# Performance work log

Hardware: AMD Instinct MI355X
Metric: run time of the kernel (lower is better)

## Reference

```python
import jax, jax.numpy as jnp
import numpy as np

B, S, IN_DIM, P_DIM, H = 2, 2048, 1024, 512, 8
HD = P_DIM // H
N_PENTA = 1024
SCALES = (128, 256, 512)
K_NEIGH = max(16, min(int(S * 0.15), 128))  # adaptive window -> 128
SCALE = 1.0 / float(np.sqrt(HD))
EPS = 1e-5


def _ln(x, g, b):
    mu = jnp.mean(x, axis=-1, keepdims=True)
    var = jnp.mean((x - mu) ** 2, axis=-1, keepdims=True)
    return (x - mu) * jax.lax.rsqrt(var + EPS) * g + b


def setup_inputs() -> dict:
    key = jax.random.key(0)
    ks = list(jax.random.split(key, 6 + 2 * len(SCALES)))
    w = lambda k, shp: jax.random.normal(k, shp, jnp.float32) * 0.02
    inp = {
        'sequence_features': jax.random.normal(ks[0], (B, S, IN_DIM), jnp.float32),
        'shared_pentachora': jax.random.normal(ks[1], (N_PENTA, 5, P_DIM), jnp.float32),
        'shared_positions': jax.random.uniform(ks[2], (N_PENTA,), dtype=jnp.float32),
        'proj_W': w(ks[3], (IN_DIM, P_DIM)), 'proj_b': jnp.zeros((P_DIM,), jnp.float32),
        'ln_g': jnp.ones((P_DIM,), jnp.float32), 'ln_b': jnp.zeros((P_DIM,), jnp.float32),
        'qkv_W': w(ks[4], (P_DIM, 3 * P_DIM)), 'qkv_b': jnp.zeros((3 * P_DIM,), jnp.float32),
        'out_W': w(ks[5], (P_DIM, P_DIM)), 'out_b': jnp.zeros((P_DIM,), jnp.float32),
    }
    i = 6
    for s in SCALES:
        inp[f'w1_{s}'] = w(ks[i], (P_DIM, 2 * s)); inp[f'b1_{s}'] = jnp.zeros((2 * s,), jnp.float32)
        inp[f'g_{s}'] = jnp.ones((2 * s,), jnp.float32); inp[f'bb_{s}'] = jnp.zeros((2 * s,), jnp.float32)
        inp[f'w2_{s}'] = w(ks[i + 1], (2 * s, s)); inp[f'b2_{s}'] = jnp.zeros((s,), jnp.float32)
        i += 2
    return inp


def _attend_one(z_b, pos_b, qkv_W, qkv_b, out_W, out_b):
    # z_b: [S, P_DIM], pos_b: [S]
    qkv = (z_b @ qkv_W + qkv_b).reshape(S, 3, H, HD)
    q = jnp.transpose(qkv[:, 0], (1, 0, 2))  # [H, S, HD]
    k = jnp.transpose(qkv[:, 1], (1, 0, 2))
    v = jnp.transpose(qkv[:, 2], (1, 0, 2))
    dist = jnp.abs(pos_b[:, None] - pos_b[None, :])  # [S, S]
    _, routes = jax.lax.top_k(-dist, K_NEIGH)        # [S, K] nearest in Cantor space
    kg = k[:, routes, :]  # [H, S, K, HD] gathered keys
    vg = v[:, routes, :]
    scores = jnp.einsum('hqd,hqkd->hqk', q, kg) * SCALE
    attn = jax.nn.softmax(scores, axis=-1)
    out = jnp.einsum('hqk,hqkd->hqd', attn, vg)
    out = jnp.transpose(out, (1, 0, 2)).reshape(S, P_DIM)
    return out @ out_W + out_b


def reference(sequence_features, shared_pentachora, shared_positions, proj_W, proj_b, ln_g, ln_b, qkv_W, qkv_b, out_W, out_b, w1_128, b1_128, g_128, bb_128, w2_128, b2_128, w1_256, b1_256, g_256, bb_256, w2_256, b2_256, w1_512, b1_512, g_512, bb_512, w2_512, b2_512):
    # centroids from pentachora vertices, L2-normalized
    cent = shared_pentachora.mean(axis=1)
    cent = cent / jnp.clip(jnp.linalg.norm(cent, axis=-1, keepdims=True), 1e-12)
    # input projection -> LN -> GELU -> L2 normalize
    z = jax.nn.gelu(_ln(sequence_features @ proj_W + proj_b, ln_g, ln_b), approximate=False)
    z = z / jnp.clip(jnp.linalg.norm(z, axis=-1, keepdims=True), 1e-12)
    # match to opinion anchors, inherit Cantor positions
    anchor_ids = jnp.argmax(jnp.einsum('bnd,pd->bnp', z, cent), axis=-1)  # [B, S]
    cantor_positions = shared_positions[anchor_ids]  # [B, S]
    # per-sample geometric sparse attention (vmapped over batch)
    z_att = jax.vmap(_attend_one, in_axes=(0, 0, None, None, None, None))(
        z, cantor_positions, qkv_W, qkv_b, out_W, out_b)  # [B, S, P_DIM]
    pooled = z_att.mean(axis=1)  # [B, P_DIM] (no attention mask)
    scale_params = (
        (w1_128, b1_128, g_128, bb_128, w2_128, b2_128),
        (w1_256, b1_256, g_256, bb_256, w2_256, b2_256),
        (w1_512, b1_512, g_512, bb_512, w2_512, b2_512),
    )
    outs = []
    for (w1, b1, g, bb, w2, b2) in scale_params:
        h = jax.nn.gelu(_ln(pooled @ w1 + b1, g, bb), approximate=False)
        outs.append(h @ w2 + b2)
    return jnp.concatenate(outs, axis=-1)  # [B, 128+256+512] concatenated scale opinions
```

## Files before the change

### kernel.cpp

```cpp
#include <hip/hip_runtime.h>
#include <math.h>

#define DEV __device__ __forceinline__

static constexpr int S_LEN  = 2048;
static constexpr int IN_DIM = 1024;
static constexpr int P_DIM  = 512;
static constexpr int NHEAD  = 8;
static constexpr int HD     = 64;
static constexpr int KN     = 128;

typedef __attribute__((ext_vector_type(8))) short bf16x8;
typedef __attribute__((ext_vector_type(4))) float f32x4;

DEV float gelu_exact(float x) {
    return 0.5f * x * (1.0f + erff(x * 0.70710678118654752440f));
}

DEV short bf_hi(float x) {
    unsigned u = __float_as_uint(x);
    unsigned r = (u + 0x7fffu + ((u >> 16) & 1u)) >> 16;
    return (short)r;
}
DEV float bf_f(short h) { return __uint_as_float(((unsigned)(unsigned short)h) << 16); }

DEV float block_reduce_sum(float v, float* sm4) {
    #pragma unroll
    for (int off = 32; off; off >>= 1) v += __shfl_down(v, off, 64);
    int lane = threadIdx.x & 63, w = threadIdx.x >> 6;
    __syncthreads();
    if (lane == 0) sm4[w] = v;
    __syncthreads();
    return sm4[0] + sm4[1] + sm4[2] + sm4[3];
}

__global__ __launch_bounds__(256) void k_split(const float* __restrict__ X,
                                               short* __restrict__ Xh,
                                               short* __restrict__ Xl) {
    long base = ((long)blockIdx.x * 256 + threadIdx.x) * 16;
    #pragma unroll
    for (int u = 0; u < 4; u++) {
        float4 v = *(const float4*)(X + base + u * 4);
        short h0 = bf_hi(v.x), h1 = bf_hi(v.y), h2 = bf_hi(v.z), h3 = bf_hi(v.w);
        *(short4*)(Xh + base + u * 4) = make_short4(h0, h1, h2, h3);
        *(short4*)(Xl + base + u * 4) =
            make_short4(bf_hi(v.x - bf_f(h0)), bf_hi(v.y - bf_f(h1)),
                        bf_hi(v.z - bf_f(h2)), bf_hi(v.w - bf_f(h3)));
    }
}

__global__ __launch_bounds__(256) void k_cent(const float* __restrict__ penta,
                                              short* __restrict__ ch,
                                              short* __restrict__ cl) {
    int p = blockIdx.x, t = threadIdx.x;
    __shared__ float sm4[4];
    float c0 = 0.f, c1 = 0.f;
    #pragma unroll
    for (int v = 0; v < 5; v++) {
        const float* row = penta + ((long)p * 5 + v) * P_DIM;
        c0 += row[t];
        c1 += row[t + 256];
    }
    c0 /= 5.0f; c1 /= 5.0f;
    float tot = block_reduce_sum(c0 * c0 + c1 * c1, sm4);
    float n = fmaxf(sqrtf(tot), 1e-12f);
    float v0 = c0 / n, v1 = c1 / n;
    short h0 = bf_hi(v0), h1 = bf_hi(v1);
    ch[p * P_DIM + t]       = h0;
    ch[p * P_DIM + t + 256] = h1;
    cl[p * P_DIM + t]       = bf_hi(v0 - bf_f(h0));
    cl[p * P_DIM + t + 256] = bf_hi(v1 - bf_f(h1));
}

template <int K, int N>
__global__ __launch_bounds__(256) void k_wt(const float* __restrict__ W,
                                            short* __restrict__ WTh,
                                            short* __restrict__ WTl) {
    __shared__ float tile[64][65];
    int bk = blockIdx.x, bn = blockIdx.y;
    int t = threadIdx.x;
    int c = t & 63, r4 = t >> 6;
    #pragma unroll
    for (int i = 0; i < 16; i++) {
        int row = r4 + i * 4;
        tile[row][c] = W[(long)(bk * 64 + row) * N + bn * 64 + c];
    }
    __syncthreads();
    #pragma unroll
    for (int i = 0; i < 16; i++) {
        int n = r4 + i * 4;
        float v = tile[c][n];
        short h = bf_hi(v);
        long o = (long)(bn * 64 + n) * K + bk * 64 + c;
        WTh[o] = h;
        WTl[o] = bf_hi(v - bf_f(h));
    }
}

template <int BM, int K, int N, int EPI>
__global__ __launch_bounds__(256) void k_mm(const short* __restrict__ Ash,
                                            const short* __restrict__ Asl,
                                            const short* __restrict__ BTh,
                                            const short* __restrict__ BTl,
                                            const float* __restrict__ bias,
                                            float* __restrict__ C,
                                            unsigned long long* __restrict__ rowkey) {
    constexpr int TI  = BM / 32;
    constexpr int CA  = BM / 8;
    constexpr int NCH = 2 * CA + 32;
    __shared__ __align__(128) short AhS[BM * 64], AlS[BM * 64];
    __shared__ __align__(128) short BhS[128 * 64], BlS[128 * 64];
    int t = threadIdx.x;
    int lane = t & 63, wave = t >> 6;
    int wr = (wave >> 1) * (BM / 2), wc = (wave & 1) * 64;
    int m = lane & 15, quad = lane >> 4;
    int rb = blockIdx.x * BM, cb = blockIdx.y * 128;
    int r8 = lane >> 3, p8 = lane & 7;
    int sl = p8 ^ r8;

    f32x4 acc[TI][4];
    #pragma unroll
    for (int i = 0; i < TI; i++)
        #pragma unroll
        for (int j = 0; j < 4; j++) acc[i][j] = (f32x4){0.f, 0.f, 0.f, 0.f};

    for (int k0 = 0; k0 < K; k0 += 64) {
        __syncthreads();
        for (int c = wave; c < NCH; c += 4) {
            const short* src; short* dst;
            if (c < CA) {
                src = Ash + (long)(rb + c * 8 + r8) * K + k0 + sl * 8;
                dst = AhS + c * 512;
            } else if (c < 2 * CA) {
                int cc = c - CA;
                src = Asl + (long)(rb + cc * 8 + r8) * K + k0 + sl * 8;
                dst = AlS + cc * 512;
            } else if (c < 2 * CA + 16) {
                int cc = c - 2 * CA;
                src = BTh + (long)(cb + cc * 8 + r8) * K + k0 + sl * 8;
                dst = BhS + cc * 512;
            } else {
                int cc = c - 2 * CA - 16;
                src = BTl + (long)(cb + cc * 8 + r8) * K + k0 + sl * 8;
                dst = BlS + cc * 512;
            }
            __builtin_amdgcn_global_load_lds(
                (const __attribute__((address_space(1))) unsigned int*)src,
                (__attribute__((address_space(3))) unsigned int*)dst, 16, 0, 0);
        }
        __syncthreads();

        #pragma unroll
        for (int ks = 0; ks < 2; ks++) {
            int so = ((ks * 4 + quad) ^ (m & 7)) * 8;
            bf16x8 ah[TI], al[TI], bh[4], bl[4];
            #pragma unroll
            for (int i = 0; i < TI; i++) {
                int off = (wr + i * 16 + m) * 64 + so;
                ah[i] = *(const bf16x8*)(AhS + off);
                al[i] = *(const bf16x8*)(AlS + off);
            }
            #pragma unroll
            for (int j = 0; j < 4; j++) {
                int off = (wc + j * 16 + m) * 64 + so;
                bh[j] = *(const bf16x8*)(BhS + off);
                bl[j] = *(const bf16x8*)(BlS + off);
            }
            #pragma unroll
            for (int i = 0; i < TI; i++)
                #pragma unroll
                for (int j = 0; j < 4; j++) {
                    acc[i][j] = __builtin_amdgcn_mfma_f32_16x16x32_bf16(ah[i], bh[j], acc[i][j], 0, 0, 0);
                    acc[i][j] = __builtin_amdgcn_mfma_f32_16x16x32_bf16(ah[i], bl[j], acc[i][j], 0, 0, 0);
                    acc[i][j] = __builtin_amdgcn_mfma_f32_16x16x32_bf16(al[i], bh[j], acc[i][j], 0, 0, 0);
                }
        }
    }

    if (EPI == 0) {
        #pragma unroll
        for (int i = 0; i < TI; i++) {
            int gr0 = rb + wr + i * 16 + quad * 4;
            #pragma unroll
            for (int j = 0; j < 4; j++) {
                int gc = cb + wc + j * 16 + m;
                float bv = bias[gc];
                #pragma unroll
                for (int r = 0; r < 4; r++)
                    C[(long)(gr0 + r) * N + gc] = acc[i][j][r] + bv;
            }
        }
    } else {
        #pragma unroll
        for (int i = 0; i < TI; i++) {
            #pragma unroll
            for (int r = 0; r < 4; r++) {
                int gr = rb + wr + i * 16 + quad * 4 + r;
                float bv = acc[i][0][r];
                int bp = cb + wc + m;
                #pragma unroll
                for (int j = 1; j < 4; j++) {
                    float v = acc[i][j][r];
                    int p = cb + wc + j * 16 + m;
                    if (v > bv) { bv = v; bp = p; }
                }
                #pragma unroll
                for (int off = 1; off < 16; off <<= 1) {
                    float ov = __shfl_xor(bv, off, 64);
                    int op = __shfl_xor(bp, off, 64);
                    if (ov > bv || (ov == bv && op < bp)) { bv = ov; bp = op; }
                }
                if (m == 0) {
                    unsigned u = __float_as_uint(bv);
                    u = (u & 0x80000000u) ? ~u : (u | 0x80000000u);
                    unsigned long long key =
                        ((unsigned long long)u << 32) | (unsigned)(0xFFFFFFFFu - (unsigned)bp);
                    atomicMax(&rowkey[gr], key);
                }
            }
        }
    }
}

__global__ __launch_bounds__(256) void k_ln_gelu_norm(const float* __restrict__ Zin,
                                                      const float* __restrict__ g,
                                                      const float* __restrict__ b,
                                                      short* __restrict__ z_h,
                                                      short* __restrict__ z_l) {
    long row = blockIdx.x;
    int t = threadIdx.x;
    __shared__ float sm4[4];
    float x0 = Zin[row * P_DIM + t], x1 = Zin[row * P_DIM + t + 256];
    float mu = block_reduce_sum(x0 + x1, sm4) * (1.0f / P_DIM);
    float d0 = x0 - mu, d1 = x1 - mu;
    float var = block_reduce_sum(d0 * d0 + d1 * d1, sm4) * (1.0f / P_DIM);
    float rs = 1.0f / sqrtf(var + 1e-5f);
    float y0 = gelu_exact(d0 * rs * g[t] + b[t]);
    float y1 = gelu_exact(d1 * rs * g[t + 256] + b[t + 256]);
    float nn = block_reduce_sum(y0 * y0 + y1 * y1, sm4);
    float n = fmaxf(sqrtf(nn), 1e-12f);
    float v0 = y0 / n, v1 = y1 / n;
    short h0 = bf_hi(v0), h1 = bf_hi(v1);
    z_h[row * P_DIM + t]       = h0;
    z_h[row * P_DIM + t + 256] = h1;
    z_l[row * P_DIM + t]       = bf_hi(v0 - bf_f(h0));
    z_l[row * P_DIM + t + 256] = bf_hi(v1 - bf_f(h1));
}

__global__ __launch_bounds__(1024) void k_sort(const unsigned long long* __restrict__ rowkey,
                                               const float* __restrict__ spos,
                                               int* __restrict__ order,
                                               float* __restrict__ pos_srt) {
    int b = blockIdx.x, t = threadIdx.x;
    __shared__ unsigned long long key[2048];
    for (int u = 0; u < 2; u++) {
        int i = t + u * 1024;
        unsigned p = 0xFFFFFFFFu - (unsigned)(rowkey[b * 2048 + i] & 0xFFFFFFFFull);
        float pv = spos[p];
        key[i] = (((unsigned long long)__float_as_uint(pv)) << 32) | (unsigned)i;
    }
    __syncthreads();
    for (int k = 2; k <= 2048; k <<= 1) {
        for (int j = k >> 1; j > 0; j >>= 1) {
            for (int u = 0; u < 2; u++) {
                int i = t + u * 1024;
                int l = i ^ j;
                if (l > i) {
                    bool up = ((i & k) == 0);
                    unsigned long long a = key[i], c = key[l];
                    if ((a > c) == up) { key[i] = c; key[l] = a; }
                }
            }
            __syncthreads();
        }
    }
    for (int u = 0; u < 2; u++) {
        int r = t + u * 1024;
        unsigned long long kk = key[r];
        order[b * 2048 + r]   = (int)(kk & 0xffffffffu);
        pos_srt[b * 2048 + r] = __uint_as_float((unsigned)(kk >> 32));
    }
}

__global__ __launch_bounds__(256) void k_routes(const float* __restrict__ pos_srt,
                                                const int* __restrict__ order,
                                                unsigned long long* __restrict__ bmG,
                                                uint2* __restrict__ bounds) {
    int blk = blockIdx.x;
    int b = blk >> 9;
    int t = threadIdx.x;
    int lane = t & 63, wave = t >> 6;
    int r = (blk & 511) * 4 + wave;
    __shared__ float ps[2048];
    __shared__ unsigned short tk[2048];
    for (int u = 0; u < 8; u++) {
        int i = t + u * 256;
        ps[i] = pos_srt[b * 2048 + i];
        tk[i] = (unsigned short)order[b * 2048 + i];
    }
    __syncthreads();

    float pi = ps[r];
    float T = 3e38f;
    #pragma unroll
    for (int a2 = 0; a2 < 2; a2++) {
        int a = lane + a2 * 64;
        int jl = r - a, jr = r + 127 - a;
        if (jl >= 0 && jr <= 2047) {
            float dl = (a > 0)   ? (pi - ps[jl]) : 0.f;
            float dr = (a < 127) ? (ps[jr] - pi) : 0.f;
            T = fminf(T, fmaxf(dl, dr));
        }
    }
    #pragma unroll
    for (int off = 1; off < 64; off <<= 1) T = fminf(T, __shfl_xor(T, off, 64));

    int lo = 0, hi = r;
    while (lo < hi) { int mid = (lo + hi) >> 1; if (pi - ps[mid] <= T) hi = mid; else lo = mid + 1; }
    int mn = lo;
    lo = r; hi = 2047;
    while (lo < hi) { int mid = (lo + hi + 1) >> 1; if (ps[mid] - pi <= T) lo = mid; else hi = mid - 1; }
    int mx = lo;
    int Ls, Rs;
    if (T > 0.f) {
        lo = 0; hi = r;
        while (lo < hi) { int mid = (lo + hi) >> 1; if (pi - ps[mid] < T) hi = mid; else lo = mid + 1; }
        Ls = lo;
        lo = r; hi = 2047;
        while (lo < hi) { int mid = (lo + hi + 1) >> 1; if (ps[mid] - pi < T) lo = mid; else hi = mid - 1; }
        Rs = lo;
    } else { Ls = r + 1; Rs = r - 1; }

    int cnt_strict = (Rs >= Ls) ? (Rs - Ls + 1) : 0;
    int need = 128 - cnt_strict;
    int l0a, l0b, r0a, r0b;
    if (cnt_strict > 0) { l0a = mn; l0b = Ls - 1; r0a = Rs + 1; r0b = mx; }
    else                { l0a = mn; l0b = mx;     r0a = 1;      r0b = 0; }
    int nL = (l0b >= l0a) ? (l0b - l0a + 1) : 0;
    int nR = (r0b >= r0a) ? (r0b - r0a + 1) : 0;
    int tiecount = nL + nR;

    int X = 65535;
    if (need < tiecount) {
        int lo2 = 0, hi2 = 2047;
        while (lo2 < hi2) {
            int mid = (lo2 + hi2) >> 1;
            int cnt = 0;
            for (int e = lane; e < tiecount; e += 64) {
                int j = (e < nL) ? (l0a + e) : (r0a + e - nL);
                cnt += (tk[j] <= mid) ? 1 : 0;
            }
            #pragma unroll
            for (int off = 1; off < 64; off <<= 1) cnt += __shfl_xor(cnt, off, 64);
            if (cnt >= need) hi2 = mid; else lo2 = mid + 1;
        }
        X = lo2;
    }

    int qlo_loc = 1 << 30, qhi_loc = -1;
    if (lane < 32) {
        unsigned long long bits = 0;
        int j0 = lane << 6, j1 = j0 + 63;
        if (cnt_strict > 0) {
            int a0 = max(Ls, j0), a1 = min(Rs, j1);
            if (a0 <= a1) {
                int s = a0 - j0, e = a1 - j0;
                unsigned long long msk = (e - s == 63) ? ~0ull
                                       : (((1ull << (e - s + 1)) - 1) << s);
                bits |= msk;
            }
        }
        int a0 = max(l0a, j0), a1 = min(l0b, j1);
        for (int j = a0; j <= a1; j++) if (tk[j] <= X) bits |= 1ull << (j - j0);
        a0 = max(r0a, j0); a1 = min(r0b, j1);
        for (int j = a0; j <= a1; j++) if (tk[j] <= X) bits |= 1ull << (j - j0);
        if (bits) {
            qlo_loc = j0 + __builtin_ctzll(bits);
            qhi_loc = j0 + 63 - __builtin_clzll(bits);
        }
        bmG[((long)(b * 2048 + r)) * 32 + lane] = bits;
    }
    #pragma unroll
    for (int off = 1; off < 64; off <<= 1) {
        qlo_loc = min(qlo_loc, __shfl_xor(qlo_loc, off, 64));
        qhi_loc = max(qhi_loc, __shfl_xor(qhi_loc, off, 64));
    }
    if (lane == 0)
        bounds[b * 2048 + r] = make_uint2((unsigned)qlo_loc, (unsigned)qhi_loc);
}

__global__ __launch_bounds__(256) void k_kprep(const float* __restrict__ qkv,
                                               const int* __restrict__ order,
                                               short* __restrict__ Ks_h,
                                               short* __restrict__ Ks_l) {
    int b = blockIdx.y;
    int t = threadIdx.x;
    int lr = t >> 5;
    int seg = t & 31;
    int rank = blockIdx.x * 8 + lr;
    int tok = order[b * 2048 + rank];
    const float4* src = (const float4*)qkv + (long)(b * 2048 + tok) * 384 + 128 + seg * 4;
    long dsto = (long)(b * 2048 + rank) * 512 + seg * 16;
    #pragma unroll
    for (int u = 0; u < 4; u++) {
        float4 v = src[u];
        short h0 = bf_hi(v.x), h1 = bf_hi(v.y), h2 = bf_hi(v.z), h3 = bf_hi(v.w);
        *(short4*)(Ks_h + dsto + u * 4) = make_short4(h0, h1, h2, h3);
        *(short4*)(Ks_l + dsto + u * 4) =
            make_short4(bf_hi(v.x - bf_f(h0)), bf_hi(v.y - bf_f(h1)),
                        bf_hi(v.z - bf_f(h2)), bf_hi(v.w - bf_f(h3)));
    }
}

__global__ __launch_bounds__(256) void k_vprep(const float* __restrict__ qkv,
                                               const int* __restrict__ order,
                                               short* __restrict__ Vt_h) {
    __shared__ short tile[64][72];
    int rt = blockIdx.x, dt = blockIdx.y, b = blockIdx.z;
    int t = threadIdx.x;
    int lr = t >> 2;
    int q4 = t & 3;
    int tok = order[b * 2048 + rt * 64 + lr];
    const float4* src = (const float4*)qkv + (long)(b * 2048 + tok) * 384 + 256 + dt * 16;
    #pragma unroll
    for (int u = 0; u < 4; u++) {
        float4 v = src[q4 + u * 4];
        int d0 = (q4 + u * 4) * 4;
        tile[d0 + 0][lr] = bf_hi(v.x);
        tile[d0 + 1][lr] = bf_hi(v.y);
        tile[d0 + 2][lr] = bf_hi(v.z);
        tile[d0 + 3][lr] = bf_hi(v.w);
    }
    __syncthreads();
    int d = t >> 2, c4 = t & 3;
    long o = ((long)(b * 512 + dt * 64 + d)) * 2048 + rt * 64 + c4 * 16;
    #pragma unroll
    for (int j = 0; j < 4; j++)
        *(short4*)(Vt_h + o + j * 4) = make_short4(tile[d][c4 * 16 + j * 4 + 0],
                                                   tile[d][c4 * 16 + j * 4 + 1],
                                                   tile[d][c4 * 16 + j * 4 + 2],
                                                   tile[d][c4 * 16 + j * 4 + 3]);
}

__global__ __launch_bounds__(256) void k_attn(const float* __restrict__ qkv,
                                              const int* __restrict__ order,
                                              const unsigned long long* __restrict__ bmG,
                                              const uint2* __restrict__ bounds,
                                              const short* __restrict__ Ks_h,
                                              const short* __restrict__ Ks_l,
                                              const short* __restrict__ Vt_h,
                                              float* __restrict__ pooledZ) {
    __shared__ __align__(16) char smem[17280];
    short* Pt = (short*)smem;
    unsigned short* cm = (unsigned short*)(smem + 10240);
    float* Opart = (float*)smem;
    float2* ml = (float2*)(smem + 16384);
    int* sh_tok = (int*)(smem + 16896);
    int* sh_lohi = (int*)(smem + 16960);
    float2* sc = (float2*)(smem + 16968);

    int gb = blockIdx.x;
    int b  = gb >> 9;
    int qg = (gb >> 2) & 127;
    int hp = gb & 3;
    int h0 = hp * 2;
    int r0 = qg * 16;
    int t = threadIdx.x;
    int lane = t & 63, wave = t >> 6;
    int rh = wave & 1, hs = wave >> 1;
    int key = lane & 15, quad = lane >> 4;

    const float4* qkvF4 = (const float4*)qkv;

    if (t < 16) sh_tok[t] = order[b * 2048 + r0 + t];
    if (t == 0) { sh_lohi[0] = 1 << 30; sh_lohi[1] = 0; }
    #pragma unroll
    for (int u = 0; u < 8; u++) {
        int e = t + u * 256;
        int c = e >> 4, q = e & 15;
        cm[c * 16 + q] = (unsigned short)(
            (bmG[((long)(b * 2048 + r0 + q)) * 32 + (c >> 2)] >> ((c & 3) * 16)) & 0xFFFF);
    }
    __syncthreads();
    if (t < 16) {
        uint2 bd = bounds[b * 2048 + r0 + t];
        atomicMin(&sh_lohi[0], (int)bd.x);
        atomicMax(&sh_lohi[1], (int)bd.y);
    }

    bf16x8 qh[2], ql[2];
    {
        long tq = (long)(b * 2048 + sh_tok[key]) * 384;
        #pragma unroll
        for (int ks = 0; ks < 2; ks++) {
            float4 v0 = qkvF4[tq + (h0 + hs) * 16 + ks * 8 + quad * 2];
            float4 v1 = qkvF4[tq + (h0 + hs) * 16 + ks * 8 + quad * 2 + 1];
            float vv[8] = {v0.x, v0.y, v0.z, v0.w, v1.x, v1.y, v1.z, v1.w};
            #pragma unroll
            for (int j = 0; j < 8; j++) {
                short hb = bf_hi(vv[j]);
                qh[ks][j] = hb;
                ql[ks][j] = bf_hi(vv[j] - bf_f(hb));
            }
        }
    }
    __syncthreads();
    int lo = sh_lohi[0] & ~63, hi = sh_lohi[1] + 1;

    float mrow[4], lrow[4];
    f32x4 Ont[4];
    #pragma unroll
    for (int r = 0; r < 4; r++) { mrow[r] = -1e30f; lrow[r] = 0.f; }
    #pragma unroll
    for (int nt = 0; nt < 4; nt++) Ont[nt] = (f32x4){0.f, 0.f, 0.f, 0.f};

    short* PtH = Pt + wave * 1280;
    short* PtL = PtH + 640;

    int hd = h0 + hs;
    long kbase = ((long)b * 2048) * 512 + hd * 64 + quad * 8;
    long vbase = ((long)(b * 512 + hd * 64 + key)) * 2048;

    for (int c0 = lo; c0 < hi; c0 += 64) {
        int cb = c0 + rh * 32;
        if (cb >= hi) continue;
        int ch0 = cb >> 4;
        unsigned long long m0 = *(const unsigned long long*)(cm + ch0 * 16 + quad * 4);
        unsigned long long m1 = (ch0 + 1 < 128)
            ? *(const unsigned long long*)(cm + (ch0 + 1) * 16 + quad * 4) : 0ull;
        if (!__any((m0 | m1) != 0ull)) continue;

        long kr0 = kbase + (long)(cb + key) * 512;
        long kr1 = kbase + (long)(cb + 16 + key) * 512;

        f32x4 S0 = (f32x4){0.f,0.f,0.f,0.f}, S1 = (f32x4){0.f,0.f,0.f,0.f};
        #pragma unroll
        for (int ks = 0; ks < 2; ks++) {
            bf16x8 b0h = *(const bf16x8*)(Ks_h + kr0 + ks * 32);
            bf16x8 b0l = *(const bf16x8*)(Ks_l + kr0 + ks * 32);
            bf16x8 b1h = *(const bf16x8*)(Ks_h + kr1 + ks * 32);
            bf16x8 b1l = *(const bf16x8*)(Ks_l + kr1 + ks * 32);
            S0 = __builtin_amdgcn_mfma_f32_16x16x32_bf16(qh[ks], b0h, S0, 0, 0, 0);
            S0 = __builtin_amdgcn_mfma_f32_16x16x32_bf16(qh[ks], b0l, S0, 0, 0, 0);
            S0 = __builtin_amdgcn_mfma_f32_16x16x32_bf16(ql[ks], b0h, S0, 0, 0, 0);
            S1 = __builtin_amdgcn_mfma_f32_16x16x32_bf16(qh[ks], b1h, S1, 0, 0, 0);
            S1 = __builtin_amdgcn_mfma_f32_16x16x32_bf16(qh[ks], b1l, S1, 0, 0, 0);
            S1 = __builtin_amdgcn_mfma_f32_16x16x32_bf16(ql[ks], b1h, S1, 0, 0, 0);
        }
        float s0[4], s1[4], p0[4], p1[4];
        unsigned bit0[4], bit1[4];
        #pragma unroll
        for (int r = 0; r < 4; r++) {
            bit0[r] = (unsigned)((m0 >> (r * 16 + key)) & 1);
            bit1[r] = (unsigned)((m1 >> (r * 16 + key)) & 1);
            s0[r] = bit0[r] ? S0[r] * 0.125f : -1e30f;
            s1[r] = bit1[r] ? S1[r] * 0.125f : -1e30f;
        }
        #pragma unroll
        for (int r = 0; r < 4; r++) {
            float cmax = fmaxf(s0[r], s1[r]);
            cmax = fmaxf(cmax, __shfl_xor(cmax, 1, 64));
            cmax = fmaxf(cmax, __shfl_xor(cmax, 2, 64));
            cmax = fmaxf(cmax, __shfl_xor(cmax, 4, 64));
            cmax = fmaxf(cmax, __shfl_xor(cmax, 8, 64));
            float mn = fmaxf(mrow[r], cmax);
            float alpha = __expf(mrow[r] - mn);
            mrow[r] = mn;
            p0[r] = bit0[r] ? __expf(s0[r] - mn) : 0.f;
            p1[r] = bit1[r] ? __expf(s1[r] - mn) : 0.f;
            float rs = p0[r] + p1[r];
            rs += __shfl_xor(rs, 1, 64);
            rs += __shfl_xor(rs, 2, 64);
            rs += __shfl_xor(rs, 4, 64);
            rs += __shfl_xor(rs, 8, 64);
            lrow[r] = lrow[r] * alpha + rs;
            #pragma unroll
            for (int nt = 0; nt < 4; nt++) Ont[nt][r] *= alpha;
        }
        #pragma unroll
        for (int r = 0; r < 4; r++) {
            short ha = bf_hi(p0[r]);
            PtH[(quad * 4 + r) * 40 + key] = ha;
            PtL[(quad * 4 + r) * 40 + key] = bf_hi(p0[r] - bf_f(ha));
            short hb = bf_hi(p1[r]);
            PtH[(quad * 4 + r) * 40 + 16 + key] = hb;
            PtL[(quad * 4 + r) * 40 + 16 + key] = bf_hi(p1[r] - bf_f(hb));
        }
        bf16x8 pfh = *(const bf16x8*)(PtH + key * 40 + quad * 8);
        bf16x8 pfl = *(const bf16x8*)(PtL + key * 40 + quad * 8);
        #pragma unroll
        for (int nt = 0; nt < 4; nt++) {
            bf16x8 vf = *(const bf16x8*)(Vt_h + vbase + (long)nt * 16 * 2048
                                         + cb + quad * 8);
            Ont[nt] = __builtin_amdgcn_mfma_f32_16x16x32_bf16(pfh, vf, Ont[nt], 0, 0, 0);
            Ont[nt] = __builtin_amdgcn_mfma_f32_16x16x32_bf16(pfl, vf, Ont[nt], 0, 0, 0);
        }
    }

    if (key == 0) {
        #pragma unroll
        for (int r = 0; r < 4; r++)
            ml[(rh * 2 + hs) * 16 + quad * 4 + r] = make_float2(mrow[r], lrow[r]);
    }
    __syncthreads();
    #pragma unroll
    for (int nt = 0; nt < 4; nt++)
        #pragma unroll
        for (int r = 0; r < 4; r++)
            Opart[rh * 2048 + (quad * 4 + r) * 128 + hs * 64 + nt * 16 + key] = Ont[nt][r];

    if (t < 32) {
        int q = t >> 1, hs2 = t & 1;
        float2 a = ml[(0 * 2 + hs2) * 16 + q];
        float2 c = ml[(1 * 2 + hs2) * 16 + q];
        float M = fmaxf(a.x, c.x);
        float w0 = __expf(a.x - M), w1 = __expf(c.x - M);
        float inv = 1.0f / fmaxf(a.y * w0 + c.y * w1, 1e-37f);
        sc[hs2 * 16 + q] = make_float2(w0 * inv, w1 * inv);
    }
    __syncthreads();

    if (t < 128) {
        int d = t, hs2 = d >> 6;
        float s = 0.f;
        #pragma unroll
        for (int q = 0; q < 16; q++) {
            float2 w = sc[hs2 * 16 + q];
            s += Opart[q * 128 + d] * w.x + Opart[2048 + q * 128 + d] * w.y;
        }
        atomicAdd(&pooledZ[b * P_DIM + h0 * HD + d], s);
    }
}

__global__ __launch_bounds__(256) void k_opool(const float* __restrict__ pooledZ,
                                               const float* __restrict__ outW,
                                               const float* __restrict__ outb,
                                               float* __restrict__ pooled) {
    int b = blockIdx.y, t = threadIdx.x;
    int c = blockIdx.x * 256 + t;
    __shared__ float pz[P_DIM];
    pz[t]       = pooledZ[b * P_DIM + t];
    pz[t + 256] = pooledZ[b * P_DIM + t + 256];
    __syncthreads();
    float acc = 0.f;
    #pragma unroll 8
    for (int d = 0; d < P_DIM; d++) acc = fmaf(pz[d], outW[d * P_DIM + c], acc);
    pooled[b * P_DIM + c] = acc + (float)S_LEN * outb[c];
}

__global__ __launch_bounds__(256) void k_exp_fc1(const float* __restrict__ pooled,
                                                 const float* __restrict__ w1_0, const float* __restrict__ b1_0,
                                                 const float* __restrict__ w1_1, const float* __restrict__ b1_1,
                                                 const float* __restrict__ w1_2, const float* __restrict__ b1_2,
                                                 float* __restrict__ h) {
    int t = threadIdx.x, b = blockIdx.y;
    int c = blockIdx.x * 256 + t;
    __shared__ float pl[P_DIM];
    pl[t]       = pooled[b * P_DIM + t]       * (1.0f / S_LEN);
    pl[t + 256] = pooled[b * P_DIM + t + 256] * (1.0f / S_LEN);
    __syncthreads();

    const float* wp; const float* bp; int s2, j;
    if (c < 256)      { wp = w1_0; bp = b1_0; s2 = 256;  j = c; }
    else if (c < 768) { wp = w1_1; bp = b1_1; s2 = 512;  j = c - 256; }
    else              { wp = w1_2; bp = b1_2; s2 = 1024; j = c - 768; }

    const float* p = wp + j;
    float acc = 0.f;
    #pragma unroll 16
    for (int k = 0; k < P_DIM; k++) {
        acc = fmaf(pl[k], *p, acc);
        p += s2;
    }
    h[(long)b * 1792 + c] = acc + bp[j];
}

__global__ __launch_bounds__(256) void k_exp_ln(float* __restrict__ h,
                                                const float* __restrict__ g0, const float* __restrict__ bb0,
                                                const float* __restrict__ g1, const float* __restrict__ bb1,
                                                const float* __restrict__ g2, const float* __restrict__ bb2) {
    int e = blockIdx.x, b = blockIdx.y, t = threadIdx.x;
    __shared__ float sm4[4];
    const int offs[3] = {0, 256, 768};
    const int ns[3]   = {256, 512, 1024};
    const float* gs[3]  = {g0, g1, g2};
    const float* bbs[3] = {bb0, bb1, bb2};
    int n = ns[e];
    float* hp = h + (long)b * 1792 + offs[e];
    const float* g = gs[e]; const float* bb = bbs[e];

    float x[4];
    float loc = 0.f;
    for (int u = 0; u < 4; u++) {
        int j = t + u * 256;
        x[u] = (j < n) ? hp[j] : 0.f;
        loc += x[u];
    }
    float mu = block_reduce_sum(loc, sm4) / (float)n;
    loc = 0.f;
    for (int u = 0; u < 4; u++) {
        int j = t + u * 256;
        if (j < n) { float d = x[u] - mu; loc += d * d; }
    }
    float var = block_reduce_sum(loc, sm4) / (float)n;
    float rs = 1.0f / sqrtf(var + 1e-5f);
    for (int u = 0; u < 4; u++) {
        int j = t + u * 256;
        if (j < n) hp[j] = gelu_exact((x[u] - mu) * rs * g[j] + bb[j]);
    }
}

__global__ __launch_bounds__(256) void k_exp_fc2(const float* __restrict__ h,
                                                 const float* __restrict__ w2_0, const float* __restrict__ b2_0,
                                                 const float* __restrict__ w2_1, const float* __restrict__ b2_1,
                                                 const float* __restrict__ w2_2, const float* __restrict__ b2_2,
                                                 float* __restrict__ out) {
    int t = threadIdx.x, b = blockIdx.y;
    int c = blockIdx.x * 256 + t;
    __shared__ float hs[1792];
    for (int u = 0; u < 7; u++) hs[t + u * 256] = h[(long)b * 1792 + t + u * 256];
    __syncthreads();
    if (c >= 896) return;

    const float* wp; const float* bp; int s2, sN, j, off_h;
    if (c < 128)      { wp = w2_0; bp = b2_0; s2 = 256;  sN = 128; j = c;       off_h = 0; }
    else if (c < 384) { wp = w2_1; bp = b2_1; s2 = 512;  sN = 256; j = c - 128; off_h = 256; }
    else              { wp = w2_2; bp = b2_2; s2 = 1024; sN = 512; j = c - 384; off_h = 768; }

    const float* p = wp + j;
    const float* hh = hs + off_h;
    float acc = 0.f;
    #pragma unroll 16
    for (int k = 0; k < s2; k++) {
        acc = fmaf(hh[k], *p, acc);
        p += sN;
    }
    out[b * 896 + c] = acc + bp[j];
}

extern "C" void kernel_launch(void* const* d_in, const int* in_sizes, int n_in,
                              void* d_out, int out_size, void* d_ws, size_t ws_size,
                              hipStream_t stream) {
    const float* seq   = (const float*)d_in[0];
    const float* penta = (const float*)d_in[1];
    const float* spos  = (const float*)d_in[2];
    const float* projW = (const float*)d_in[3];
    const float* projb = (const float*)d_in[4];
    const float* lng   = (const float*)d_in[5];
    const float* lnb   = (const float*)d_in[6];
    const float* qkvW  = (const float*)d_in[7];
    const float* qkvb  = (const float*)d_in[8];
    const float* outW  = (const float*)d_in[9];
    const float* outb  = (const float*)d_in[10];

    float* ws      = (float*)d_ws;
    float* z_pre   = ws;
    short* z_h     = (short*)(z_pre + 2097152);
    short* z_l     = z_h + 2097152;
    float* qkv     = (float*)(z_l + 2097152);
    float* pooledZ = qkv + 6291456;
    float* pooled  = pooledZ + 4096;
    float* hbuf    = pooled + 1024;
    unsigned long long* rowkey = (unsigned long long*)(hbuf + 4096);
    float* pos_srt = (float*)(rowkey + 4096);
    int*   order   = (int*)(pos_srt + 4096);
    uint2* bounds  = (uint2*)(order + 4096);
    unsigned long long* bmG = (unsigned long long*)(bounds + 4096);
    short* cent_h  = (short*)(bmG + 131072);
    short* cent_l  = cent_h + 524288;
    short* pjWT_h  = cent_l + 524288;
    short* pjWT_l  = pjWT_h + 524288;
    short* qkWT_h  = pjWT_l + 524288;
    short* qkWT_l  = qkWT_h + 786432;

    short* seq_h = (short*)qkv;
    short* seq_l = seq_h + 4194304;
    short* Ks_h = (short*)z_pre;
    short* Ks_l = Ks_h + 2097152;
    short* Vt_h = cent_h;

    k_cent<<<1024, 256, 0, stream>>>(penta, cent_h, cent_l);
    { dim3 g(16, 8);  k_wt<IN_DIM, P_DIM><<<g, 256, 0, stream>>>(projW, pjWT_h, pjWT_l); }
    { dim3 g(8, 24);  k_wt<P_DIM, 3 * P_DIM><<<g, 256, 0, stream>>>(qkvW, qkWT_h, qkWT_l); }
    k_split<<<1024, 256, 0, stream>>>(seq, seq_h, seq_l);

    { dim3 g(64, 4);  k_mm<64, IN_DIM, P_DIM, 0><<<g, 256, 0, stream>>>(
          seq_h, seq_l, pjWT_h, pjWT_l, projb, z_pre, nullptr); }
    k_ln_gelu_norm<<<4096, 256, 0, stream>>>(z_pre, lng, lnb, z_h, z_l);

    hipMemsetAsync(rowkey, 0, 4096 * sizeof(unsigned long long), stream);
    hipMemsetAsync(pooledZ, 0, 1024 * sizeof(float), stream);
    { dim3 g(32, 8);  k_mm<128, P_DIM, 1024, 1><<<g, 256, 0, stream>>>(
          z_h, z_l, cent_h, cent_l, nullptr, nullptr, rowkey); }
    k_sort<<<2, 1024, 0, stream>>>(rowkey, spos, order, pos_srt);

    { dim3 g(32, 12); k_mm<128, P_DIM, 3 * P_DIM, 0><<<g, 256, 0, stream>>>(
          z_h, z_l, qkWT_h, qkWT_l, qkvb, qkv, nullptr); }
    k_routes<<<1024, 256, 0, stream>>>(pos_srt, order, bmG, bounds);
    { dim3 g(256, 2); k_kprep<<<g, 256, 0, stream>>>(qkv, order, Ks_h, Ks_l); }
    { dim3 g(32, 8, 2); k_vprep<<<g, 256, 0, stream>>>(qkv, order, Vt_h); }
    k_attn<<<1024, 256, 0, stream>>>(qkv, order, bmG, bounds,
                                     Ks_h, Ks_l, Vt_h, pooledZ);

    { dim3 g(2, 2); k_opool<<<g, 256, 0, stream>>>(pooledZ, outW, outb, pooled); }

    dim3 g1(7, 2);
    k_exp_fc1<<<g1, 256, 0, stream>>>(pooled,
        (const float*)d_in[11], (const float*)d_in[12],
        (const float*)d_in[17], (const float*)d_in[18],
        (const float*)d_in[23], (const float*)d_in[24], hbuf);
    dim3 g2(3, 2);
    k_exp_ln<<<g2, 256, 0, stream>>>(hbuf,
        (const float*)d_in[13], (const float*)d_in[14],
        (const float*)d_in[19], (const float*)d_in[20],
        (const float*)d_in[25], (const float*)d_in[26]);
    dim3 g3(4, 2);
    k_exp_fc2<<<g3, 256, 0, stream>>>(hbuf,
        (const float*)d_in[15], (const float*)d_in[16],
        (const float*)d_in[21], (const float*)d_in[22],
        (const float*)d_in[27], (const float*)d_in[28], (float*)d_out);
}
```

Measured before the change: 393.3 us.

## Merge prep, K/V prep and tail kernels; replace bitonic sort with rank counting

Several small launches are folded into fewer kernels. The centroid, weight-transpose and input-split kernels plus the two memsets become one prep kernel, K and V prep become one, and the out-projection and expert MLP stages become a single 1024-thread tail kernel. The 2-block bitonic sort is replaced by a 16-block rank-by-counting kernel, where each thread compares its key against all 2048 keys, removing 66 barrier stages. This cuts launch and serialization overhead, at the cost of a single-block-per-batch tail with low parallelism and O(n^2) comparisons in the rank kernel.

```diff
diff --git a/kernel.cpp b/kernel.cpp
--- a/kernel.cpp
+++ b/kernel.cpp
@@ -34,50 +34,9 @@
     return sm4[0] + sm4[1] + sm4[2] + sm4[3];
 }
 
-__global__ __launch_bounds__(256) void k_split(const float* __restrict__ X,
-                                               short* __restrict__ Xh,
-                                               short* __restrict__ Xl) {
-    long base = ((long)blockIdx.x * 256 + threadIdx.x) * 16;
-    #pragma unroll
-    for (int u = 0; u < 4; u++) {
-        float4 v = *(const float4*)(X + base + u * 4);
-        short h0 = bf_hi(v.x), h1 = bf_hi(v.y), h2 = bf_hi(v.z), h3 = bf_hi(v.w);
-        *(short4*)(Xh + base + u * 4) = make_short4(h0, h1, h2, h3);
-        *(short4*)(Xl + base + u * 4) =
-            make_short4(bf_hi(v.x - bf_f(h0)), bf_hi(v.y - bf_f(h1)),
-                        bf_hi(v.z - bf_f(h2)), bf_hi(v.w - bf_f(h3)));
-    }
-}
-
-__global__ __launch_bounds__(256) void k_cent(const float* __restrict__ penta,
-                                              short* __restrict__ ch,
-                                              short* __restrict__ cl) {
-    int p = blockIdx.x, t = threadIdx.x;
-    __shared__ float sm4[4];
-    float c0 = 0.f, c1 = 0.f;
-    #pragma unroll
-    for (int v = 0; v < 5; v++) {
-        const float* row = penta + ((long)p * 5 + v) * P_DIM;
-        c0 += row[t];
-        c1 += row[t + 256];
-    }
-    c0 /= 5.0f; c1 /= 5.0f;
-    float tot = block_reduce_sum(c0 * c0 + c1 * c1, sm4);
-    float n = fmaxf(sqrtf(tot), 1e-12f);
-    float v0 = c0 / n, v1 = c1 / n;
-    short h0 = bf_hi(v0), h1 = bf_hi(v1);
-    ch[p * P_DIM + t]       = h0;
-    ch[p * P_DIM + t + 256] = h1;
-    cl[p * P_DIM + t]       = bf_hi(v0 - bf_f(h0));
-    cl[p * P_DIM + t + 256] = bf_hi(v1 - bf_f(h1));
-}
-
-template <int K, int N>
-__global__ __launch_bounds__(256) void k_wt(const float* __restrict__ W,
-                                            short* __restrict__ WTh,
-                                            short* __restrict__ WTl) {
-    __shared__ float tile[64][65];
-    int bk = blockIdx.x, bn = blockIdx.y;
+DEV void wt_body(const float* __restrict__ W, short* __restrict__ WTh,
+                 short* __restrict__ WTl, int K, int N, int bk, int bn,
+                 float (*tile)[65]) {
     int t = threadIdx.x;
     int c = t & 63, r4 = t >> 6;
     #pragma unroll
@@ -94,6 +53,59 @@
         long o = (long)(bn * 64 + n) * K + bk * 64 + c;
         WTh[o] = h;
         WTl[o] = bf_hi(v - bf_f(h));
+    }
+}
+
+__global__ __launch_bounds__(256) void k_prep(const float* __restrict__ penta,
+                                              short* __restrict__ ch, short* __restrict__ cl,
+                                              const float* __restrict__ projW,
+                                              short* __restrict__ pjh, short* __restrict__ pjl,
+                                              const float* __restrict__ qkvW,
+                                              short* __restrict__ qkh, short* __restrict__ qkl,
+                                              const float* __restrict__ seq,
+                                              short* __restrict__ sh, short* __restrict__ sl,
+                                              unsigned long long* __restrict__ rowkey,
+                                              float* __restrict__ pooledZ) {
+    __shared__ float tile[64][65];
+    __shared__ float sm4[4];
+    int blk = blockIdx.x, t = threadIdx.x;
+    if (blk < 1024) {
+        int p = blk;
+        if (t < 4) rowkey[p * 4 + t] = 0ull;
+        if (p < 4) pooledZ[p * 256 + t] = 0.f;
+        float c0 = 0.f, c1 = 0.f;
+        #pragma unroll
+        for (int v = 0; v < 5; v++) {
+            const float* row = penta + ((long)p * 5 + v) * P_DIM;
+            c0 += row[t];
+            c1 += row[t + 256];
+        }
+        c0 /= 5.0f; c1 /= 5.0f;
+        float tot = block_reduce_sum(c0 * c0 + c1 * c1, sm4);
+        float n = fmaxf(sqrtf(tot), 1e-12f);
+        float v0 = c0 / n, v1 = c1 / n;
+        short h0 = bf_hi(v0), h1 = bf_hi(v1);
+        ch[p * P_DIM + t]       = h0;
+        ch[p * P_DIM + t + 256] = h1;
+        cl[p * P_DIM + t]       = bf_hi(v0 - bf_f(h0));
+        cl[p * P_DIM + t + 256] = bf_hi(v1 - bf_f(h1));
+    } else if (blk < 1152) {
+        int id = blk - 1024;
+        wt_body(projW, pjh, pjl, IN_DIM, P_DIM, id & 15, id >> 4, tile);
+    } else if (blk < 1344) {
+        int id = blk - 1152;
+        wt_body(qkvW, qkh, qkl, P_DIM, 3 * P_DIM, id & 7, id >> 3, tile);
+    } else {
+        long base = ((long)(blk - 1344) * 256 + t) * 16;
+        #pragma unroll
+        for (int u = 0; u < 4; u++) {
+            float4 v = *(const float4*)(seq + base + u * 4);
+            short h0 = bf_hi(v.x), h1 = bf_hi(v.y), h2 = bf_hi(v.z), h3 = bf_hi(v.w);
+            *(short4*)(sh + base + u * 4) = make_short4(h0, h1, h2, h3);
+            *(short4*)(sl + base + u * 4) =
+                make_short4(bf_hi(v.x - bf_f(h0)), bf_hi(v.y - bf_f(h1)),
+                            bf_hi(v.z - bf_f(h2)), bf_hi(v.w - bf_f(h3)));
+        }
     }
 }
 
@@ -247,39 +259,25 @@
     z_l[row * P_DIM + t + 256] = bf_hi(v1 - bf_f(h1));
 }
 
-__global__ __launch_bounds__(1024) void k_sort(const unsigned long long* __restrict__ rowkey,
-                                               const float* __restrict__ spos,
-                                               int* __restrict__ order,
-                                               float* __restrict__ pos_srt) {
-    int b = blockIdx.x, t = threadIdx.x;
+__global__ __launch_bounds__(256) void k_rank(const unsigned long long* __restrict__ rowkey,
+                                              const float* __restrict__ spos,
+                                              int* __restrict__ order,
+                                              float* __restrict__ pos_srt) {
+    int b = blockIdx.y, t = threadIdx.x;
     __shared__ unsigned long long key[2048];
-    for (int u = 0; u < 2; u++) {
-        int i = t + u * 1024;
+    for (int u = 0; u < 8; u++) {
+        int i = t + u * 256;
         unsigned p = 0xFFFFFFFFu - (unsigned)(rowkey[b * 2048 + i] & 0xFFFFFFFFull);
-        float pv = spos[p];
-        key[i] = (((unsigned long long)__float_as_uint(pv)) << 32) | (unsigned)i;
-    }
-    __syncthreads();
-    for (int k = 2; k <= 2048; k <<= 1) {
-        for (int j = k >> 1; j > 0; j >>= 1) {
-            for (int u = 0; u < 2; u++) {
-                int i = t + u * 1024;
-                int l = i ^ j;
-                if (l > i) {
-                    bool up = ((i & k) == 0);
-                    unsigned long long a = key[i], c = key[l];
-                    if ((a > c) == up) { key[i] = c; key[l] = a; }
-                }
-            }
-            __syncthreads();
-        }
-    }
-    for (int u = 0; u < 2; u++) {
-        int r = t + u * 1024;
-        unsigned long long kk = key[r];
-        order[b * 2048 + r]   = (int)(kk & 0xffffffffu);
-        pos_srt[b * 2048 + r] = __uint_as_float((unsigned)(kk >> 32));
-    }
+        key[i] = (((unsigned long long)__float_as_uint(spos[p])) << 32) | (unsigned)i;
+    }
+    __syncthreads();
+    int i = blockIdx.x * 256 + t;
+    unsigned long long ki = key[i];
+    int rank = 0;
+    #pragma unroll 8
+    for (int j = 0; j < 2048; j++) rank += (key[j] < ki) ? 1 : 0;
+    order[b * 2048 + rank]   = i;
+    pos_srt[b * 2048 + rank] = __uint_as_float((unsigned)(ki >> 32));
 }
 
 __global__ __launch_bounds__(256) void k_routes(const float* __restrict__ pos_srt,
@@ -389,57 +387,56 @@
         bounds[b * 2048 + r] = make_uint2((unsigned)qlo_loc, (unsigned)qhi_loc);
 }
 
-__global__ __launch_bounds__(256) void k_kprep(const float* __restrict__ qkv,
-                                               const int* __restrict__ order,
-                                               short* __restrict__ Ks_h,
-                                               short* __restrict__ Ks_l) {
-    int b = blockIdx.y;
-    int t = threadIdx.x;
-    int lr = t >> 5;
-    int seg = t & 31;
-    int rank = blockIdx.x * 8 + lr;
-    int tok = order[b * 2048 + rank];
-    const float4* src = (const float4*)qkv + (long)(b * 2048 + tok) * 384 + 128 + seg * 4;
-    long dsto = (long)(b * 2048 + rank) * 512 + seg * 16;
-    #pragma unroll
-    for (int u = 0; u < 4; u++) {
-        float4 v = src[u];
-        short h0 = bf_hi(v.x), h1 = bf_hi(v.y), h2 = bf_hi(v.z), h3 = bf_hi(v.w);
-        *(short4*)(Ks_h + dsto + u * 4) = make_short4(h0, h1, h2, h3);
-        *(short4*)(Ks_l + dsto + u * 4) =
-            make_short4(bf_hi(v.x - bf_f(h0)), bf_hi(v.y - bf_f(h1)),
-                        bf_hi(v.z - bf_f(h2)), bf_hi(v.w - bf_f(h3)));
-    }
-}
-
-__global__ __launch_bounds__(256) void k_vprep(const float* __restrict__ qkv,
-                                               const int* __restrict__ order,
-                                               short* __restrict__ Vt_h) {
+__global__ __launch_bounds__(256) void k_kv(const float* __restrict__ qkv,
+                                            const int* __restrict__ order,
+                                            short* __restrict__ Ks_h,
+                                            short* __restrict__ Ks_l,
+                                            short* __restrict__ Vt_h) {
     __shared__ short tile[64][72];
-    int rt = blockIdx.x, dt = blockIdx.y, b = blockIdx.z;
-    int t = threadIdx.x;
-    int lr = t >> 2;
-    int q4 = t & 3;
-    int tok = order[b * 2048 + rt * 64 + lr];
-    const float4* src = (const float4*)qkv + (long)(b * 2048 + tok) * 384 + 256 + dt * 16;
-    #pragma unroll
-    for (int u = 0; u < 4; u++) {
-        float4 v = src[q4 + u * 4];
-        int d0 = (q4 + u * 4) * 4;
-        tile[d0 + 0][lr] = bf_hi(v.x);
-        tile[d0 + 1][lr] = bf_hi(v.y);
-        tile[d0 + 2][lr] = bf_hi(v.z);
-        tile[d0 + 3][lr] = bf_hi(v.w);
-    }
-    __syncthreads();
-    int d = t >> 2, c4 = t & 3;
-    long o = ((long)(b * 512 + dt * 64 + d)) * 2048 + rt * 64 + c4 * 16;
-    #pragma unroll
-    for (int j = 0; j < 4; j++)
-        *(short4*)(Vt_h + o + j * 4) = make_short4(tile[d][c4 * 16 + j * 4 + 0],
-                                                   tile[d][c4 * 16 + j * 4 + 1],
-                                                   tile[d][c4 * 16 + j * 4 + 2],
-                                                   tile[d][c4 * 16 + j * 4 + 3]);
+    int blk = blockIdx.x, t = threadIdx.x;
+    if (blk < 512) {
+        int b = blk >> 8, bx = blk & 255;
+        int lr = t >> 5;
+        int seg = t & 31;
+        int rank = bx * 8 + lr;
+        int tok = order[b * 2048 + rank];
+        const float4* src = (const float4*)qkv + (long)(b * 2048 + tok) * 384 + 128 + seg * 4;
+        long dsto = (long)(b * 2048 + rank) * 512 + seg * 16;
+        #pragma unroll
+        for (int u = 0; u < 4; u++) {
+            float4 v = src[u];
+            short h0 = bf_hi(v.x), h1 = bf_hi(v.y), h2 = bf_hi(v.z), h3 = bf_hi(v.w);
+            *(short4*)(Ks_h + dsto + u * 4) = make_short4(h0, h1, h2, h3);
+            *(short4*)(Ks_l + dsto + u * 4) =
+                make_short4(bf_hi(v.x - bf_f(h0)), bf_hi(v.y - bf_f(h1)),
+                            bf_hi(v.z - bf_f(h2)), bf_hi(v.w - bf_f(h3)));
+        }
+    } else {
+        int id = blk - 512;
+        int rt = id & 31, dt = (id >> 5) & 7, b = id >> 8;
+        int lr = t >> 2;
+        int q4 = t & 3;
+        int tok = order[b * 2048 + rt * 64 + lr];
+        const float4* src = (const float4*)qkv + (long)(b * 2048 + tok) * 384 + 256 + dt * 16;
+        #pragma unroll
+        for (int u = 0; u < 4; u++) {
+            float4 v = src[q4 + u * 4];
+            int d0 = (q4 + u * 4) * 4;
+            tile[d0 + 0][lr] = bf_hi(v.x);
+            tile[d0 + 1][lr] = bf_hi(v.y);
+            tile[d0 + 2][lr] = bf_hi(v.z);
+            tile[d0 + 3][lr] = bf_hi(v.w);
+        }
+        __syncthreads();
+        int d = t >> 2, c4 = t & 3;
+        long o = ((long)(b * 512 + dt * 64 + d)) * 2048 + rt * 64 + c4 * 16;
+        #pragma unroll
+        for (int j = 0; j < 4; j++)
+            *(short4*)(Vt_h + o + j * 4) = make_short4(tile[d][c4 * 16 + j * 4 + 0],
+                                                       tile[d][c4 * 16 + j * 4 + 1],
+                                                       tile[d][c4 * 16 + j * 4 + 2],
+                                                       tile[d][c4 * 16 + j * 4 + 3]);
+    }
 }
 
 __global__ __launch_bounds__(256) void k_attn(const float* __restrict__ qkv,
@@ -632,110 +629,100 @@
     }
 }
 
-__global__ __launch_bounds__(256) void k_opool(const float* __restrict__ pooledZ,
+__global__ __launch_bounds__(1024) void k_tail(const float* __restrict__ pooledZ,
                                                const float* __restrict__ outW,
                                                const float* __restrict__ outb,
-                                               float* __restrict__ pooled) {
-    int b = blockIdx.y, t = threadIdx.x;
-    int c = blockIdx.x * 256 + t;
+                                               const float* __restrict__ w1_0, const float* __restrict__ b1_0,
+                                               const float* __restrict__ g_0,  const float* __restrict__ bb_0,
+                                               const float* __restrict__ w2_0, const float* __restrict__ b2_0,
+                                               const float* __restrict__ w1_1, const float* __restrict__ b1_1,
+                                               const float* __restrict__ g_1,  const float* __restrict__ bb_1,
+                                               const float* __restrict__ w2_1, const float* __restrict__ b2_1,
+                                               const float* __restrict__ w1_2, const float* __restrict__ b1_2,
+                                               const float* __restrict__ g_2,  const float* __restrict__ bb_2,
+                                               const float* __restrict__ w2_2, const float* __restrict__ b2_2,
+                                               float* __restrict__ out) {
     __shared__ float pz[P_DIM];
-    pz[t]       = pooledZ[b * P_DIM + t];
-    pz[t + 256] = pooledZ[b * P_DIM + t + 256];
-    __syncthreads();
-    float acc = 0.f;
-    #pragma unroll 8
-    for (int d = 0; d < P_DIM; d++) acc = fmaf(pz[d], outW[d * P_DIM + c], acc);
-    pooled[b * P_DIM + c] = acc + (float)S_LEN * outb[c];
-}
-
-__global__ __launch_bounds__(256) void k_exp_fc1(const float* __restrict__ pooled,
-                                                 const float* __restrict__ w1_0, const float* __restrict__ b1_0,
-                                                 const float* __restrict__ w1_1, const float* __restrict__ b1_1,
-                                                 const float* __restrict__ w1_2, const float* __restrict__ b1_2,
-                                                 float* __restrict__ h) {
-    int t = threadIdx.x, b = blockIdx.y;
-    int c = blockIdx.x * 256 + t;
     __shared__ float pl[P_DIM];
-    pl[t]       = pooled[b * P_DIM + t]       * (1.0f / S_LEN);
-    pl[t + 256] = pooled[b * P_DIM + t + 256] * (1.0f / S_LEN);
-    __syncthreads();
-
-    const float* wp; const float* bp; int s2, j;
-    if (c < 256)      { wp = w1_0; bp = b1_0; s2 = 256;  j = c; }
-    else if (c < 768) { wp = w1_1; bp = b1_1; s2 = 512;  j = c - 256; }
-    else              { wp = w1_2; bp = b1_2; s2 = 1024; j = c - 768; }
-
-    const float* p = wp + j;
-    float acc = 0.f;
-    #pragma unroll 16
-    for (int k = 0; k < P_DIM; k++) {
-        acc = fmaf(pl[k], *p, acc);
-        p += s2;
-    }
-    h[(long)b * 1792 + c] = acc + bp[j];
-}
-
-__global__ __launch_bounds__(256) void k_exp_ln(float* __restrict__ h,
-                                                const float* __restrict__ g0, const float* __restrict__ bb0,
-                                                const float* __restrict__ g1, const float* __restrict__ bb1,
-                                                const float* __restrict__ g2, const float* __restrict__ bb2) {
-    int e = blockIdx.x, b = blockIdx.y, t = threadIdx.x;
-    __shared__ float sm4[4];
+    __shared__ float hs[1792];
+    __shared__ float red[16];
+    __shared__ float mvs[2];
+    int b = blockIdx.x, t = threadIdx.x;
+
+    if (t < 512) pz[t] = pooledZ[b * P_DIM + t];
+    __syncthreads();
+    if (t < 512) {
+        float acc = 0.f;
+        #pragma unroll 8
+        for (int d = 0; d < P_DIM; d++) acc = fmaf(pz[d], outW[d * P_DIM + t], acc);
+        pl[t] = (acc + (float)S_LEN * outb[t]) * (1.0f / S_LEN);
+    }
+    __syncthreads();
+
+    for (int c = t; c < 1792; c += 1024) {
+        const float* wp; const float* bp; int s2; int j;
+        if (c < 256)      { wp = w1_0; bp = b1_0; s2 = 256;  j = c; }
+        else if (c < 768) { wp = w1_1; bp = b1_1; s2 = 512;  j = c - 256; }
+        else              { wp = w1_2; bp = b1_2; s2 = 1024; j = c - 768; }
+        const float* p = wp + j;
+        float acc = 0.f;
+        #pragma unroll 16
+        for (int k = 0; k < P_DIM; k++) { acc = fmaf(pl[k], *p, acc); p += s2; }
+        hs[c] = acc + bp[j];
+    }
+    __syncthreads();
+
     const int offs[3] = {0, 256, 768};
     const int ns[3]   = {256, 512, 1024};
-    const float* gs[3]  = {g0, g1, g2};
-    const float* bbs[3] = {bb0, bb1, bb2};
-    int n = ns[e];
-    float* hp = h + (long)b * 1792 + offs[e];
-    const float* g = gs[e]; const float* bb = bbs[e];
-
-    float x[4];
-    float loc = 0.f;
-    for (int u = 0; u < 4; u++) {
-        int j = t + u * 256;
-        x[u] = (j < n) ? hp[j] : 0.f;
-        loc += x[u];
-    }
-    float mu = block_reduce_sum(loc, sm4) / (float)n;
-    loc = 0.f;
-    for (int u = 0; u < 4; u++) {
-        int j = t + u * 256;
-        if (j < n) { float d = x[u] - mu; loc += d * d; }
-    }
-    float var = block_reduce_sum(loc, sm4) / (float)n;
-    float rs = 1.0f / sqrtf(var + 1e-5f);
-    for (int u = 0; u < 4; u++) {
-        int j = t + u * 256;
-        if (j < n) hp[j] = gelu_exact((x[u] - mu) * rs * g[j] + bb[j]);
-    }
-}
-
-__global__ __launch_bounds__(256) void k_exp_fc2(const float* __restrict__ h,
-                                                 const float* __restrict__ w2_0, const float* __restrict__ b2_0,
-                                                 const float* __restrict__ w2_1, const float* __restrict__ b2_1,
-                                                 const float* __restrict__ w2_2, const float* __restrict__ b2_2,
-                                                 float* __restrict__ out) {
-    int t = threadIdx.x, b = blockIdx.y;
-    int c = blockIdx.x * 256 + t;
-    __shared__ float hs[1792];
-    for (int u = 0; u < 7; u++) hs[t + u * 256] = h[(long)b * 1792 + t + u * 256];
-    __syncthreads();
-    if (c >= 896) return;
-
-    const float* wp; const float* bp; int s2, sN, j, off_h;
-    if (c < 128)      { wp = w2_0; bp = b2_0; s2 = 256;  sN = 128; j = c;       off_h = 0; }
-    else if (c < 384) { wp = w2_1; bp = b2_1; s2 = 512;  sN = 256; j = c - 128; off_h = 256; }
-    else              { wp = w2_2; bp = b2_2; s2 = 1024; sN = 512; j = c - 384; off_h = 768; }
-
-    const float* p = wp + j;
-    const float* hh = hs + off_h;
-    float acc = 0.f;
-    #pragma unroll 16
-    for (int k = 0; k < s2; k++) {
-        acc = fmaf(hh[k], *p, acc);
-        p += sN;
-    }
-    out[b * 896 + c] = acc + bp[j];
+    const float* gsv[3]  = {g_0, g_1, g_2};
+    const float* bbs[3]  = {bb_0, bb_1, bb_2};
+    #pragma unroll
+    for (int e = 0; e < 3; e++) {
+        int off = offs[e], n = ns[e];
+        float v = (t < n) ? hs[off + t] : 0.f;
+        float s = v;
+        #pragma unroll
+        for (int o = 32; o; o >>= 1) s += __shfl_down(s, o, 64);
+        if ((t & 63) == 0) red[t >> 6] = s;
+        __syncthreads();
+        if (t == 0) {
+            float a = 0.f;
+            #pragma unroll
+            for (int w = 0; w < 16; w++) a += red[w];
+            mvs[0] = a / (float)n;
+        }
+        __syncthreads();
+        float mu = mvs[0];
+        float d = (t < n) ? v - mu : 0.f;
+        s = d * d;
+        #pragma unroll
+        for (int o = 32; o; o >>= 1) s += __shfl_down(s, o, 64);
+        if ((t & 63) == 0) red[t >> 6] = s;
+        __syncthreads();
+        if (t == 0) {
+            float a = 0.f;
+            #pragma unroll
+            for (int w = 0; w < 16; w++) a += red[w];
+            mvs[1] = 1.0f / sqrtf(a / (float)n + 1e-5f);
+        }
+        __syncthreads();
+        float rs = mvs[1];
+        if (t < n) hs[off + t] = gelu_exact(d * rs * gsv[e][t] + bbs[e][t]);
+        __syncthreads();
+    }
+
+    if (t < 896) {
+        const float* wp; const float* bp; int s2, sN, j, off_h;
+        if (t < 128)      { wp = w2_0; bp = b2_0; s2 = 256;  sN = 128; j = t;       off_h = 0; }
+        else if (t < 384) { wp = w2_1; bp = b2_1; s2 = 512;  sN = 256; j = t - 128; off_h = 256; }
+        else              { wp = w2_2; bp = b2_2; s2 = 1024; sN = 512; j = t - 384; off_h = 768; }
+        const float* p = wp + j;
+        const float* hh = hs + off_h;
+        float acc = 0.f;
+        #pragma unroll 16
+        for (int k = 0; k < s2; k++) { acc = fmaf(hh[k], *p, acc); p += sN; }
+        out[b * 896 + t] = acc + bp[j];
+    }
 }
 
 extern "C" void kernel_launch(void* const* d_in, const int* in_sizes, int n_in,
@@ -779,44 +766,35 @@
     short* Ks_l = Ks_h + 2097152;
     short* Vt_h = cent_h;
 
-    k_cent<<<1024, 256, 0, stream>>>(penta, cent_h, cent_l);
-    { dim3 g(16, 8);  k_wt<IN_DIM, P_DIM><<<g, 256, 0, stream>>>(projW, pjWT_h, pjWT_l); }
-    { dim3 g(8, 24);  k_wt<P_DIM, 3 * P_DIM><<<g, 256, 0, stream>>>(qkvW, qkWT_h, qkWT_l); }
-    k_split<<<1024, 256, 0, stream>>>(seq, seq_h, seq_l);
+    k_prep<<<2368, 256, 0, stream>>>(penta, cent_h, cent_l,
+                                     projW, pjWT_h, pjWT_l,
+                                     qkvW, qkWT_h, qkWT_l,
+                                     seq, seq_h, seq_l,
+                                     rowkey, pooledZ);
 
     { dim3 g(64, 4);  k_mm<64, IN_DIM, P_DIM, 0><<<g, 256, 0, stream>>>(
           seq_h, seq_l, pjWT_h, pjWT_l, projb, z_pre, nullptr); }
     k_ln_gelu_norm<<<4096, 256, 0, stream>>>(z_pre, lng, lnb, z_h, z_l);
 
-    hipMemsetAsync(rowkey, 0, 4096 * sizeof(unsigned long long), stream);
-    hipMemsetAsync(pooledZ, 0, 1024 * sizeof(float), stream);
     { dim3 g(32, 8);  k_mm<128, P_DIM, 1024, 1><<<g, 256, 0, stream>>>(
           z_h, z_l, cent_h, cent_l, nullptr, nullptr, rowkey); }
-    k_sort<<<2, 1024, 0, stream>>>(rowkey, spos, order, pos_srt);
+    { dim3 g(8, 2);   k_rank<<<g, 256, 0, stream>>>(rowkey, spos, order, pos_srt); }
 
     { dim3 g(32, 12); k_mm<128, P_DIM, 3 * P_DIM, 0><<<g, 256, 0, stream>>>(
           z_h, z_l, qkWT_h, qkWT_l, qkvb, qkv, nullptr); }
     k_routes<<<1024, 256, 0, stream>>>(pos_srt, order, bmG, bounds);
-    { dim3 g(256, 2); k_kprep<<<g, 256, 0, stream>>>(qkv, order, Ks_h, Ks_l); }
-    { dim3 g(32, 8, 2); k_vprep<<<g, 256, 0, stream>>>(qkv, order, Vt_h); }
+    k_kv<<<1024, 256, 0, stream>>>(qkv, order, Ks_h, Ks_l, Vt_h);
     k_attn<<<1024, 256, 0, stream>>>(qkv, order, bmG, bounds,
                                      Ks_h, Ks_l, Vt_h, pooledZ);
 
-    { dim3 g(2, 2); k_opool<<<g, 256, 0, stream>>>(pooledZ, outW, outb, pooled); }
-
-    dim3 g1(7, 2);
-    k_exp_fc1<<<g1, 256, 0, stream>>>(pooled,
+    k_tail<<<2, 1024, 0, stream>>>(pooledZ, outW, outb,
         (const float*)d_in[11], (const float*)d_in[12],
+        (const float*)d_in[13], (const float*)d_in[14],
+        (const float*)d_in[15], (const float*)d_in[16],
         (const float*)d_in[17], (const float*)d_in[18],
-        (const float*)d_in[23], (const float*)d_in[24], hbuf);
-    dim3 g2(3, 2);
-    k_exp_ln<<<g2, 256, 0, stream>>>(hbuf,
-        (const float*)d_in[13], (const float*)d_in[14],
         (const float*)d_in[19], (const float*)d_in[20],
-        (const float*)d_in[25], (const float*)d_in[26]);
-    dim3 g3(4, 2);
-    k_exp_fc2<<<g3, 256, 0, stream>>>(hbuf,
-        (const float*)d_in[15], (const float*)d_in[16],
         (const float*)d_in[21], (const float*)d_in[22],
+        (const float*)d_in[23], (const float*)d_in[24],
+        (const float*)d_in[25], (const float*)d_in[26],
         (const float*)d_in[27], (const float*)d_in[28], (float*)d_out);
 }
```

After: 409.3 us. 1.04x slower.
